# Kernel tuning notes

Measured on AMD Instinct MI355X. Metric: run time of the kernel, lower is better.

The kernel has to match this reference:

```python
import jax, jax.numpy as jnp
import numpy as np
import math

HIDDEN = 1024
HEADS = 16
D_K = HIDDEN // HEADS
EPS = 1e-5


def gelu_tanh(x):
    c = math.sqrt(2.0 / math.pi)
    return 0.5 * x * (1.0 + jnp.tanh(c * (x + 0.044715 * x ** 3)))


def layer_norm(x, gamma, beta):
    mu = jnp.mean(x, axis=-1, keepdims=True)
    var = jnp.mean((x - mu) ** 2, axis=-1, keepdims=True)
    return (x - mu) * jax.lax.rsqrt(var + EPS) * gamma + beta


def setup_inputs() -> dict:
    key = jax.random.key(0)
    ks = jax.random.split(key, 12)
    s = 1.0 / math.sqrt(HIDDEN)
    s4 = 1.0 / math.sqrt(4 * HIDDEN)
    inp = {
        "x": jax.random.normal(ks[0], (2, 2048, HIDDEN), dtype=jnp.float32),
        # attention linears, stored as (in, out) so y = x @ W + b
        "Wq": jax.random.uniform(ks[1], (HIDDEN, HIDDEN), minval=-s, maxval=s),
        "bq": jax.random.uniform(ks[2], (HIDDEN,), minval=-s, maxval=s),
        "Wv": jax.random.uniform(ks[3], (HIDDEN, HIDDEN), minval=-s, maxval=s),
        "bv": jax.random.uniform(ks[4], (HIDDEN,), minval=-s, maxval=s),
        "Wo": jax.random.uniform(ks[5], (HIDDEN, HIDDEN), minval=-s, maxval=s),
        "bo": jax.random.uniform(ks[6], (HIDDEN,), minval=-s, maxval=s),
        # feed-forward
        "W1": jax.random.uniform(ks[7], (HIDDEN, 4 * HIDDEN), minval=-s, maxval=s),
        "b1": jax.random.uniform(ks[8], (4 * HIDDEN,), minval=-s, maxval=s),
        "W2": jax.random.uniform(ks[9], (4 * HIDDEN, HIDDEN), minval=-s4, maxval=s4),
        "b2": jax.random.uniform(ks[10], (HIDDEN,), minval=-s4, maxval=s4),
        # layer norms
        "g1": jnp.ones((HIDDEN,), jnp.float32),
        "beta1": jnp.zeros((HIDDEN,), jnp.float32),
        "g2": jnp.ones((HIDDEN,), jnp.float32),
        "beta2": jnp.zeros((HIDDEN,), jnp.float32),
    }
    return inp


def attention(x, Wq, bq, Wv, bv, Wo, bo):
    bs, seq, _ = x.shape
    qk = (x @ Wq + bq).reshape(bs, seq, HEADS, D_K).transpose(0, 2, 1, 3)  # b h s d
    v = (x @ Wv + bv).reshape(bs, seq, HEADS, D_K).transpose(0, 2, 1, 3)
    scores = jnp.einsum('bhqd,bhkd->bhqk', qk, qk) / math.sqrt(D_K)
    causal = jnp.tril(jnp.ones((seq, seq), dtype=bool))
    scores = jnp.where(causal[None, None], scores, -jnp.inf)
    attn = jax.nn.softmax(scores, axis=-1)
    out = jnp.einsum('bhqk,bhkd->bhqd', attn, v)
    out = out.transpose(0, 2, 1, 3).reshape(bs, seq, HIDDEN)
    return out @ Wo + bo


def reference(x, Wq, bq, Wv, bv, Wo, bo, W1, b1, W2, b2, g1, beta1, g2, beta2):
    x = x + attention(layer_norm(x, g1, beta1), Wq, bq, Wv, bv, Wo, bo)
    h = layer_norm(x, g2, beta2)
    ff = gelu_tanh(h @ W1 + b1) @ W2 + b2  # chunking is a memory detail; same math
    return x + ff
```

## Files before the change

### kernel.cpp

```cpp
#include <hip/hip_runtime.h>

typedef unsigned short u16;
typedef short bf16x8 __attribute__((ext_vector_type(8)));
typedef float f32x4 __attribute__((ext_vector_type(4)));

__device__ __forceinline__ float bf2f(u16 u) {
    union { unsigned int i; float f; } v; v.i = ((unsigned int)u) << 16; return v.f;
}
__device__ __forceinline__ u16 f2bf(float f) {
    union { float f; unsigned int i; } v; v.f = f;
    unsigned int r = v.i + 0x7fffu + ((v.i >> 16) & 1u);
    return (u16)(r >> 16);
}

__device__ __forceinline__ void gload16(const u16* g, u16* l) {
    __builtin_amdgcn_global_load_lds((__attribute__((address_space(1))) void*)(u16*)g,
                                     (__attribute__((address_space(3))) void*)l, 16, 0, 0);
}

__global__ __launch_bounds__(256) void prep(const float* __restrict__ Wq,
                                            const float* __restrict__ Wv,
                                            const float* __restrict__ Wo,
                                            const float* __restrict__ W1,
                                            const float* __restrict__ W2,
                                            const float* __restrict__ bq,
                                            const float* __restrict__ bv,
                                            u16* __restrict__ WqT, u16* __restrict__ WvT,
                                            u16* __restrict__ WoT, u16* __restrict__ W1T,
                                            u16* __restrict__ W2T, float* __restrict__ bqv) {
    int id = blockIdx.x;
    if (id >= 2816) {
        int i = (id - 2816) * 256 + threadIdx.x;
        bqv[i] = (i < 1024) ? bq[i] : bv[i - 1024];
        return;
    }
    const float* in; u16* out; int R, C, bx, by;
    if (id < 256)       { in = Wq; out = WqT; R = 1024; C = 1024; bx = id & 15;          by = id >> 4; }
    else if (id < 512)  { int t = id - 256;  in = Wv; out = WvT; R = 1024; C = 1024; bx = t & 15; by = t >> 4; }
    else if (id < 768)  { int t = id - 512;  in = Wo; out = WoT; R = 1024; C = 1024; bx = t & 15; by = t >> 4; }
    else if (id < 1792) { int t = id - 768;  in = W1; out = W1T; R = 1024; C = 4096; bx = t & 63; by = t >> 6; }
    else                { int t = id - 1792; in = W2; out = W2T; R = 4096; C = 1024; bx = t & 15; by = t >> 4; }
    __shared__ u16 tile[64][65];
    int c0 = bx * 64, r0 = by * 64;
    for (int i = threadIdx.x; i < 4096; i += 256) {
        int r = i >> 6, c = i & 63;
        tile[r][c] = f2bf(in[(size_t)(r0 + r) * C + c0 + c]);
    }
    __syncthreads();
    for (int i = threadIdx.x; i < 4096; i += 256) {
        int r = i >> 6, c = i & 63;
        out[(size_t)(c0 + r) * R + r0 + c] = tile[c][r];
    }
}

__global__ __launch_bounds__(256) void transpose_bf16_s(const u16* __restrict__ in,
                                                        u16* __restrict__ out,
                                                        int R, int C, int istride) {
    __shared__ u16 tile[64][65];
    int c0 = blockIdx.x * 64, r0 = blockIdx.y * 64;
    in  += (size_t)blockIdx.z * R * istride;
    out += (size_t)blockIdx.z * R * C;
    for (int i = threadIdx.x; i < 4096; i += 256) {
        int r = i >> 6, c = i & 63;
        tile[r][c] = in[(size_t)(r0 + r) * istride + c0 + c];
    }
    __syncthreads();
    for (int i = threadIdx.x; i < 4096; i += 256) {
        int r = i >> 6, c = i & 63;
        out[(size_t)(c0 + r) * R + r0 + c] = tile[c][r];
    }
}

__global__ __launch_bounds__(256) void ln_f32(const float* __restrict__ x,
                                              const float* __restrict__ g,
                                              const float* __restrict__ be,
                                              u16* __restrict__ out) {
    int row = blockIdx.x, tid = threadIdx.x;
    int lane = tid & 63, wave = tid >> 6;
    const float* xr = x + (size_t)row * 1024 + tid * 4;
    float4 f4 = *(const float4*)xr;
    float v[4] = {f4.x, f4.y, f4.z, f4.w};
    float s1 = v[0] + v[1] + v[2] + v[3];
    float s2 = v[0]*v[0] + v[1]*v[1] + v[2]*v[2] + v[3]*v[3];
#pragma unroll
    for (int mm = 1; mm < 64; mm <<= 1) { s1 += __shfl_xor(s1, mm); s2 += __shfl_xor(s2, mm); }
    __shared__ float a1[4], a2[4];
    if (lane == 0) { a1[wave] = s1; a2[wave] = s2; }
    __syncthreads();
    s1 = a1[0] + a1[1] + a1[2] + a1[3];
    s2 = a2[0] + a2[1] + a2[2] + a2[3];
    float mean = s1 * (1.0f / 1024.0f);
    float var  = s2 * (1.0f / 1024.0f) - mean * mean;
    float rstd = rsqrtf(var + 1e-5f);
#pragma unroll
    for (int i = 0; i < 4; ++i) {
        int c = tid * 4 + i;
        float o = (v[i] - mean) * rstd * g[c] + be[c];
        out[(size_t)row * 1024 + c] = f2bf(o);
    }
}

template <int BN, int ACT, int RES, typename OutT>
__global__ __launch_bounds__(256) void gemm_gl(const u16* __restrict__ A,
                                               const u16* __restrict__ WT,
                                               const float* __restrict__ bias,
                                               const float* __restrict__ resid,
                                               OutT* __restrict__ C,
                                               int M, int N, int K, int cpx) {
    constexpr int JN = BN / 32;
    __shared__ u16 lds_a[128 * 64];
    __shared__ u16 lds_b[BN * 64];
    int tid = threadIdx.x;
    int lane = tid & 63, wave = tid >> 6;
    int l16 = lane & 15, quad = lane >> 4;
    int wm = (wave >> 1) * 64, wn = (wave & 1) * (BN / 2);

    int id = blockIdx.x;
    int slot = id >> 3;
    int bx = (id & 7) * cpx + (slot >> 5);
    int by = slot & 31;
    int m0 = by * 128, n0 = bx * BN;
    f32x4 acc[4][JN] = {};

    int scol = ((lane & 7) ^ (lane >> 3)) * 8;
    const u16* Ab = A  + (size_t)(m0 + wave * 8 + (lane >> 3)) * K + scol;
    const u16* Bb = WT + (size_t)(n0 + wave * 8 + (lane >> 3)) * K + scol;
    u16* la = lds_a + wave * 512;
    u16* lb = lds_b + wave * 512;

    int xk = (l16 & 7);

    for (int k0 = 0; k0 < K; k0 += 64) {
        __syncthreads();
#pragma unroll
        for (int it = 0; it < 4; ++it)
            gload16(Ab + (size_t)it * 32 * K + k0, la + it * 2048);
#pragma unroll
        for (int it = 0; it < JN; ++it)
            gload16(Bb + (size_t)it * 32 * K + k0, lb + it * 2048);
        __syncthreads();
#pragma unroll
        for (int s = 0; s < 2; ++s) {
            bf16x8 af[4], bfr[JN];
#pragma unroll
            for (int i = 0; i < 4; ++i)
                af[i] = *(const bf16x8*)&lds_a[(wm + i * 16 + l16) * 64 + (((s * 4 + quad) ^ xk) * 8)];
#pragma unroll
            for (int j = 0; j < JN; ++j)
                bfr[j] = *(const bf16x8*)&lds_b[(wn + j * 16 + l16) * 64 + (((s * 4 + quad) ^ xk) * 8)];
#pragma unroll
            for (int i = 0; i < 4; ++i)
#pragma unroll
                for (int j = 0; j < JN; ++j)
                    acc[i][j] = __builtin_amdgcn_mfma_f32_16x16x32_bf16(af[i], bfr[j], acc[i][j], 0, 0, 0);
        }
    }

#pragma unroll
    for (int j = 0; j < JN; ++j) {
        int col = n0 + wn + j * 16 + l16;
        float bv = bias[col];
#pragma unroll
        for (int i = 0; i < 4; ++i) {
            int rbase = m0 + wm + i * 16 + quad * 4;
#pragma unroll
            for (int r = 0; r < 4; ++r) {
                size_t idx = (size_t)(rbase + r) * N + col;
                float v = acc[i][j][r] + bv;
                if (ACT == 1) {
                    float u = v;
                    float y = 0.7978845608028654f * (u + 0.044715f * u * u * u);
                    float t = __expf(2.0f * y);
                    float th = 1.0f - 2.0f / (t + 1.0f);
                    v = 0.5f * u * (1.0f + th);
                }
                if (RES) v += resid[idx];
                if constexpr (sizeof(OutT) == 4) C[idx] = v;
                else                             C[idx] = f2bf(v);
            }
        }
    }
}

template <int ACT>
__global__ __launch_bounds__(256, 2) void gemm_big(const u16* __restrict__ A,
                                                   const u16* __restrict__ WT,
                                                   const float* __restrict__ bias,
                                                   u16* __restrict__ C,
                                                   int M, int N, int K) {
    __shared__ u16 lds_a[256 * 64];
    __shared__ u16 lds_b[128 * 64];
    int tid = threadIdx.x;
    int lane = tid & 63, wave = tid >> 6;
    int l16 = lane & 15, quad = lane >> 4;
    int wm = (wave >> 1) * 128, wn = (wave & 1) * 64;
    int id = blockIdx.x;
    int bx = id & 31, by = id >> 5;
    int m0 = by * 256, n0 = bx * 128;
    f32x4 acc[8][4] = {};

    int scol = ((lane & 7) ^ (lane >> 3)) * 8;
    const u16* Ab = A  + (size_t)(m0 + wave * 8 + (lane >> 3)) * K + scol;
    const u16* Bb = WT + (size_t)(n0 + wave * 8 + (lane >> 3)) * K + scol;
    u16* la = lds_a + wave * 512;
    u16* lb = lds_b + wave * 512;
    int xk = (l16 & 7);

    for (int k0 = 0; k0 < K; k0 += 64) {
        __syncthreads();
#pragma unroll
        for (int it = 0; it < 8; ++it)
            gload16(Ab + (size_t)it * 32 * K + k0, la + it * 2048);
#pragma unroll
        for (int it = 0; it < 4; ++it)
            gload16(Bb + (size_t)it * 32 * K + k0, lb + it * 2048);
        __syncthreads();
#pragma unroll
        for (int s = 0; s < 2; ++s) {
            bf16x8 bfr[4];
#pragma unroll
            for (int j = 0; j < 4; ++j)
                bfr[j] = *(const bf16x8*)&lds_b[(wn + j * 16 + l16) * 64 + (((s * 4 + quad) ^ xk) * 8)];
#pragma unroll
            for (int i = 0; i < 8; ++i) {
                bf16x8 af = *(const bf16x8*)&lds_a[(wm + i * 16 + l16) * 64 + (((s * 4 + quad) ^ xk) * 8)];
#pragma unroll
                for (int j = 0; j < 4; ++j)
                    acc[i][j] = __builtin_amdgcn_mfma_f32_16x16x32_bf16(af, bfr[j], acc[i][j], 0, 0, 0);
            }
        }
    }

#pragma unroll
    for (int j = 0; j < 4; ++j) {
        int col = n0 + wn + j * 16 + l16;
        float bv = bias[col];
#pragma unroll
        for (int i = 0; i < 8; ++i) {
            int rbase = m0 + wm + i * 16 + quad * 4;
#pragma unroll
            for (int r = 0; r < 4; ++r) {
                size_t idx = (size_t)(rbase + r) * N + col;
                float v = acc[i][j][r] + bv;
                if (ACT == 1) {
                    float u = v;
                    float y = 0.7978845608028654f * (u + 0.044715f * u * u * u);
                    float t = __expf(2.0f * y);
                    float th = 1.0f - 2.0f / (t + 1.0f);
                    v = 0.5f * u * (1.0f + th);
                }
                C[idx] = f2bf(v);
            }
        }
    }
}

__global__ __launch_bounds__(256) void attn_kernel(const u16* __restrict__ QV,
                                                   const u16* __restrict__ Vt,
                                                   u16* __restrict__ Out) {
    int id = blockIdx.x;
    int slot = id >> 3;
    int hb = (id & 7) + 8 * (slot & 3);
    int p  = slot >> 2;
    int h = hb & 15, b = hb >> 4;
    int tid = threadIdx.x;
    int lane = tid & 63, wave = tid >> 6;
    int l16 = lane & 15, quad = lane >> 4;

    __shared__ u16 k_lds[64 * 64];
    __shared__ u16 v_lds[64 * 64];
    __shared__ u16 p_lds[4][16 * 72];

    bf16x8 ones;
#pragma unroll
    for (int e = 0; e < 8; ++e) ones[e] = (short)0x3F80;

    int srow = wave * 8 + (lane >> 3);
    int sc8  = ((lane & 7) ^ (lane >> 3)) * 8;
    int xk   = (l16 & 7);

    for (int half = 0; half < 2; ++half) {
        int t = half ? (31 - p) : p;
        int q0 = t * 64;

        const u16* qp = QV + ((size_t)b * 2048 + q0 + wave * 16 + l16) * 2048 + h * 64;
        bf16x8 qf[2];
        qf[0] = *(const bf16x8*)&qp[quad * 8];
        qf[1] = *(const bf16x8*)&qp[32 + quad * 8];

        f32x4 O[4] = {};
        f32x4 L = {};

        for (int kt = 0; kt <= t; ++kt) {
            const u16* kg = QV + ((size_t)b * 2048 + kt * 64 + srow) * 2048 + h * 64 + sc8;
            const u16* vg = Vt + ((((size_t)b * 16 + h) * 64) + srow) * 2048 + kt * 64 + sc8;
            __syncthreads();
            gload16(kg,                      k_lds + wave * 512);
            gload16(kg + (size_t)32 * 2048,  k_lds + wave * 512 + 2048);
            gload16(vg,                      v_lds + wave * 512);
            gload16(vg + (size_t)32 * 2048,  v_lds + wave * 512 + 2048);
            __syncthreads();

            f32x4 S[4] = {};
#pragma unroll
            for (int s = 0; s < 2; ++s)
#pragma unroll
                for (int j = 0; j < 4; ++j) {
                    bf16x8 kf = *(const bf16x8*)&k_lds[(j * 16 + l16) * 64 + (((s * 4 + quad) ^ xk) * 8)];
                    S[j] = __builtin_amdgcn_mfma_f32_16x16x32_bf16(qf[s], kf, S[j], 0, 0, 0);
                }

            if (kt == t) {
#pragma unroll
                for (int j = 0; j < 4; ++j) {
                    int key = j * 16 + l16;
#pragma unroll
                    for (int r = 0; r < 4; ++r)
                        if (key > wave * 16 + quad * 4 + r) S[j][r] = -1e30f;
                }
            }

#pragma unroll
            for (int j = 0; j < 4; ++j)
#pragma unroll
                for (int r = 0; r < 4; ++r) {
                    float pp = __expf(S[j][r] * 0.125f);
                    p_lds[wave][(quad * 4 + r) * 72 + j * 16 + l16] = f2bf(pp);
                }

#pragma unroll
            for (int s = 0; s < 2; ++s) {
                bf16x8 pf = *(const bf16x8*)&p_lds[wave][l16 * 72 + s * 32 + quad * 8];
                L = __builtin_amdgcn_mfma_f32_16x16x32_bf16(pf, ones, L, 0, 0, 0);
#pragma unroll
                for (int dj = 0; dj < 4; ++dj) {
                    bf16x8 vf = *(const bf16x8*)&v_lds[(dj * 16 + l16) * 64 + (((s * 4 + quad) ^ xk) * 8)];
                    O[dj] = __builtin_amdgcn_mfma_f32_16x16x32_bf16(pf, vf, O[dj], 0, 0, 0);
                }
            }
        }

#pragma unroll
        for (int r = 0; r < 4; ++r) {
            int qg = q0 + wave * 16 + quad * 4 + r;
            float inv = 1.0f / L[r];
#pragma unroll
            for (int dj = 0; dj < 4; ++dj)
                Out[((size_t)b * 2048 + qg) * 1024 + h * 64 + dj * 16 + l16] =
                    f2bf(O[dj][r] * inv);
        }
    }
}

extern "C" void kernel_launch(void* const* d_in, const int* in_sizes, int n_in,
                              void* d_out, int out_size, void* d_ws, size_t ws_size,
                              hipStream_t stream) {
    const float* x   = (const float*)d_in[0];
    const float* Wq  = (const float*)d_in[1];
    const float* bq  = (const float*)d_in[2];
    const float* Wv  = (const float*)d_in[3];
    const float* bv  = (const float*)d_in[4];
    const float* Wo  = (const float*)d_in[5];
    const float* bo  = (const float*)d_in[6];
    const float* W1  = (const float*)d_in[7];
    const float* b1  = (const float*)d_in[8];
    const float* W2  = (const float*)d_in[9];
    const float* b2  = (const float*)d_in[10];
    const float* g1  = (const float*)d_in[11];
    const float* be1 = (const float*)d_in[12];
    const float* g2  = (const float*)d_in[13];
    const float* be2 = (const float*)d_in[14];

    char* ws = (char*)d_ws;
    const size_t MB = 1 << 20;
    u16*   WqT  = (u16*)(ws + 0  * MB);
    u16*   WvT  = (u16*)(ws + 2  * MB);
    u16*   WoT  = (u16*)(ws + 4  * MB);
    u16*   W1T  = (u16*)(ws + 6  * MB);
    u16*   W2T  = (u16*)(ws + 14 * MB);
    u16*   h1   = (u16*)(ws + 22 * MB);
    u16*   QV   = (u16*)(ws + 30 * MB);
    float* x2   = (float*)(ws + 30 * MB);
    u16*   Vt   = (u16*)(ws + 46 * MB);
    u16*   ff1  = (u16*)(ws + 46 * MB);
    float* bqv  = (float*)(ws + 78 * MB);

    prep<<<2824, 256, 0, stream>>>(Wq, Wv, Wo, W1, W2, bq, bv,
                                   WqT, WvT, WoT, W1T, W2T, bqv);

    ln_f32<<<4096, 256, 0, stream>>>(x, g1, be1, h1);

    gemm_gl<64, 0, 0, u16><<<1024, 256, 0, stream>>>(h1, WqT, bqv, nullptr, QV, 4096, 2048, 1024, 4);

    transpose_bf16_s<<<dim3(16, 32, 2), 256, 0, stream>>>(QV + 1024, Vt, 2048, 1024, 2048);

    attn_kernel<<<512, 256, 0, stream>>>(QV, Vt, h1);

    gemm_gl<64, 0, 1, float><<<512, 256, 0, stream>>>(h1, WoT, bo, x, x2, 4096, 1024, 1024, 2);

    ln_f32<<<4096, 256, 0, stream>>>(x2, g2, be2, h1);

    gemm_big<1><<<512, 256, 0, stream>>>(h1, W1T, b1, ff1, 4096, 4096, 1024);

    gemm_gl<64, 0, 1, float><<<512, 256, 0, stream>>>(ff1, W2T, b2, x2, (float*)d_out, 4096, 1024, 4096, 2);
}
```

Baseline: 341.3 us.

## Split-K the final FF GEMM into three slices and store residual in bf16

Replaces the last FF2 GEMM (K=4096, 512 blocks of 128x64) with a 3-way split-K kernel that uses 256x128 tiles and writes bf16 partial sums, followed by an elementwise reduce kernel that adds the partials, the residual and the bias. The attention output plus residual is now stored in bf16 instead of fp32, with a matching bf16 LayerNorm kernel, which cuts memory traffic. The aim is better parallelism and reuse for the long-K GEMM. The cost is an extra launch and extra partial-sum traffic, and precision drops because partials and the residual are rounded to bf16. The workspace is also reused aggressively for the partial buffers.

Result: faster. 329.3 us (-3.5%).

```diff
diff --git a/kernel.cpp b/kernel.cpp
--- a/kernel.cpp
+++ b/kernel.cpp
@@ -100,6 +100,36 @@
     }
 }
 
+__global__ __launch_bounds__(256) void ln_bf16(const u16* __restrict__ x,
+                                               const float* __restrict__ g,
+                                               const float* __restrict__ be,
+                                               u16* __restrict__ out) {
+    int row = blockIdx.x, tid = threadIdx.x;
+    int lane = tid & 63, wave = tid >> 6;
+    u16 e[4]; *(uint2*)e = *(const uint2*)(x + (size_t)row * 1024 + tid * 4);
+    float v[4];
+#pragma unroll
+    for (int i = 0; i < 4; ++i) v[i] = bf2f(e[i]);
+    float s1 = v[0] + v[1] + v[2] + v[3];
+    float s2 = v[0]*v[0] + v[1]*v[1] + v[2]*v[2] + v[3]*v[3];
+#pragma unroll
+    for (int mm = 1; mm < 64; mm <<= 1) { s1 += __shfl_xor(s1, mm); s2 += __shfl_xor(s2, mm); }
+    __shared__ float a1[4], a2[4];
+    if (lane == 0) { a1[wave] = s1; a2[wave] = s2; }
+    __syncthreads();
+    s1 = a1[0] + a1[1] + a1[2] + a1[3];
+    s2 = a2[0] + a2[1] + a2[2] + a2[3];
+    float mean = s1 * (1.0f / 1024.0f);
+    float var  = s2 * (1.0f / 1024.0f) - mean * mean;
+    float rstd = rsqrtf(var + 1e-5f);
+#pragma unroll
+    for (int i = 0; i < 4; ++i) {
+        int c = tid * 4 + i;
+        float o = (v[i] - mean) * rstd * g[c] + be[c];
+        out[(size_t)row * 1024 + c] = f2bf(o);
+    }
+}
+
 template <int BN, int ACT, int RES, typename OutT>
 __global__ __launch_bounds__(256) void gemm_gl(const u16* __restrict__ A,
                                                const u16* __restrict__ WT,
@@ -127,7 +157,6 @@
     const u16* Bb = WT + (size_t)(n0 + wave * 8 + (lane >> 3)) * K + scol;
     u16* la = lds_a + wave * 512;
     u16* lb = lds_b + wave * 512;
-
     int xk = (l16 & 7);
 
     for (int k0 = 0; k0 < K; k0 += 64) {
@@ -253,6 +282,97 @@
             }
         }
     }
+}
+
+__global__ __launch_bounds__(256, 2) void gemm_split(const u16* __restrict__ A,
+                                                     const u16* __restrict__ WT,
+                                                     u16* __restrict__ p0,
+                                                     u16* __restrict__ p1,
+                                                     u16* __restrict__ p2,
+                                                     int M, int N, int K) {
+    __shared__ u16 lds_a[256 * 64];
+    __shared__ u16 lds_b[128 * 64];
+    int tid = threadIdx.x;
+    int lane = tid & 63, wave = tid >> 6;
+    int l16 = lane & 15, quad = lane >> 4;
+    int wm = (wave >> 1) * 128, wn = (wave & 1) * 64;
+    int id = blockIdx.x;
+    int slice = id >> 7;
+    int t = id & 127;
+    int bx = t & 7, by = t >> 3;
+    int m0 = by * 256, n0 = bx * 128;
+    int k_lo = (slice == 0) ? 0 : 64 * (22 + 21 * (slice - 1));
+    int k_hi = (slice == 2) ? K : 64 * (22 + 21 * slice);
+    u16* P = (slice == 0) ? p0 : (slice == 1) ? p1 : p2;
+    f32x4 acc[8][4] = {};
+
+    int scol = ((lane & 7) ^ (lane >> 3)) * 8;
+    const u16* Ab = A  + (size_t)(m0 + wave * 8 + (lane >> 3)) * K + scol;
+    const u16* Bb = WT + (size_t)(n0 + wave * 8 + (lane >> 3)) * K + scol;
+    u16* la = lds_a + wave * 512;
+    u16* lb = lds_b + wave * 512;
+    int xk = (l16 & 7);
+
+    for (int k0 = k_lo; k0 < k_hi; k0 += 64) {
+        __syncthreads();
+#pragma unroll
+        for (int it = 0; it < 8; ++it)
+            gload16(Ab + (size_t)it * 32 * K + k0, la + it * 2048);
+#pragma unroll
+        for (int it = 0; it < 4; ++it)
+            gload16(Bb + (size_t)it * 32 * K + k0, lb + it * 2048);
+        __syncthreads();
+#pragma unroll
+        for (int s = 0; s < 2; ++s) {
+            bf16x8 bfr[4];
+#pragma unroll
+            for (int j = 0; j < 4; ++j)
+                bfr[j] = *(const bf16x8*)&lds_b[(wn + j * 16 + l16) * 64 + (((s * 4 + quad) ^ xk) * 8)];
+#pragma unroll
+            for (int i = 0; i < 8; ++i) {
+                bf16x8 af = *(const bf16x8*)&lds_a[(wm + i * 16 + l16) * 64 + (((s * 4 + quad) ^ xk) * 8)];
+#pragma unroll
+                for (int j = 0; j < 4; ++j)
+                    acc[i][j] = __builtin_amdgcn_mfma_f32_16x16x32_bf16(af, bfr[j], acc[i][j], 0, 0, 0);
+            }
+        }
+    }
+
+#pragma unroll
+    for (int j = 0; j < 4; ++j) {
+        int col = n0 + wn + j * 16 + l16;
+#pragma unroll
+        for (int i = 0; i < 8; ++i) {
+            int rbase = m0 + wm + i * 16 + quad * 4;
+#pragma unroll
+            for (int r = 0; r < 4; ++r)
+                P[(size_t)(rbase + r) * N + col] = f2bf(acc[i][j][r]);
+        }
+    }
+}
+
+__global__ __launch_bounds__(256) void ff2_reduce(const u16* __restrict__ p0,
+                                                  const u16* __restrict__ p1,
+                                                  const u16* __restrict__ p2,
+                                                  const u16* __restrict__ x2b,
+                                                  const float* __restrict__ b2,
+                                                  float* __restrict__ out) {
+    size_t i = ((size_t)blockIdx.x * 256 + threadIdx.x) * 8;
+    int col = (int)(i & 1023);
+    uint4 a0 = *(const uint4*)&p0[i];
+    uint4 a1 = *(const uint4*)&p1[i];
+    uint4 a2 = *(const uint4*)&p2[i];
+    uint4 ax = *(const uint4*)&x2b[i];
+    const u16* e0 = (const u16*)&a0;
+    const u16* e1 = (const u16*)&a1;
+    const u16* e2 = (const u16*)&a2;
+    const u16* ex = (const u16*)&ax;
+    float o[8];
+#pragma unroll
+    for (int e = 0; e < 8; ++e)
+        o[e] = bf2f(ex[e]) + bf2f(e0[e]) + bf2f(e1[e]) + bf2f(e2[e]) + b2[col + e];
+    *(float4*)&out[i]     = *(float4*)&o[0];
+    *(float4*)&out[i + 4] = *(float4*)&o[4];
 }
 
 __global__ __launch_bounds__(256) void attn_kernel(const u16* __restrict__ QV,
@@ -380,10 +500,13 @@
     u16*   W2T  = (u16*)(ws + 14 * MB);
     u16*   h1   = (u16*)(ws + 22 * MB);
     u16*   QV   = (u16*)(ws + 30 * MB);
-    float* x2   = (float*)(ws + 30 * MB);
+    u16*   x2b  = (u16*)(ws + 30 * MB);
     u16*   Vt   = (u16*)(ws + 46 * MB);
     u16*   ff1  = (u16*)(ws + 46 * MB);
     float* bqv  = (float*)(ws + 78 * MB);
+    u16*   fp0  = (u16*)(ws + 0  * MB);
+    u16*   fp1  = (u16*)(ws + 22 * MB);
+    u16*   fp2  = (u16*)(ws + 38 * MB);
 
     prep<<<2824, 256, 0, stream>>>(Wq, Wv, Wo, W1, W2, bq, bv,
                                    WqT, WvT, WoT, W1T, W2T, bqv);
@@ -396,11 +519,13 @@
 
     attn_kernel<<<512, 256, 0, stream>>>(QV, Vt, h1);
 
-    gemm_gl<64, 0, 1, float><<<512, 256, 0, stream>>>(h1, WoT, bo, x, x2, 4096, 1024, 1024, 2);
-
-    ln_f32<<<4096, 256, 0, stream>>>(x2, g2, be2, h1);
+    gemm_gl<64, 0, 1, u16><<<512, 256, 0, stream>>>(h1, WoT, bo, x, x2b, 4096, 1024, 1024, 2);
+
+    ln_bf16<<<4096, 256, 0, stream>>>(x2b, g2, be2, h1);
 
     gemm_big<1><<<512, 256, 0, stream>>>(h1, W1T, b1, ff1, 4096, 4096, 1024);
 
-    gemm_gl<64, 0, 1, float><<<512, 256, 0, stream>>>(ff1, W2T, b2, x2, (float*)d_out, 4096, 1024, 4096, 2);
-}
+    gemm_split<<<384, 256, 0, stream>>>(ff1, W2T, fp0, fp1, fp2, 4096, 1024, 4096);
+
+    ff2_reduce<<<2048, 256, 0, stream>>>(fp0, fp1, fp2, x2b, b2, (float*)d_out);
+}
```
